# Optimization experiments

Measured on AMD Instinct MI355X. Metric: run time of the kernel, lower is better.

## Reference

```python
import jax, jax.numpy as jnp
import numpy as np
import math

B, N, D, H = 8, 1024, 512, 8
DH = D // H  # 64
FF = 4 * D   # 2048
SQRT_2_OVER_PI = math.sqrt(2.0 / math.pi)
LN_EPS = 1e-12


def gelu_new(x):
    # tanh-approx GELU as in DenseGatedGeluDense.gelu_new
    return 0.5 * x * (1.0 + jnp.tanh(SQRT_2_OVER_PI * (x + 0.044715 * x ** 3)))


def layer_norm(x, scale, bias):
    m = jnp.mean(x, axis=-1, keepdims=True)
    v = jnp.mean((x - m) ** 2, axis=-1, keepdims=True)
    return (x - m) * jax.lax.rsqrt(v + LN_EPS) * scale + bias


def setup_inputs() -> dict:
    key = jax.random.key(0)
    ks = jax.random.split(key, 12)
    w = lambda k, shape: (jax.random.normal(k, shape, jnp.float32) * 0.02)
    return {
        "X": jax.random.normal(ks[0], (B, N, D), jnp.float32),
        "train_ind": jax.random.randint(ks[1], (B, N), 0, 2).astype(jnp.int32),
        "batch_ind": jax.random.randint(ks[2], (B, N), 0, 2).astype(jnp.int32),
        "Wq": w(ks[3], (D, D)), "bq": jnp.zeros((D,), jnp.float32),
        "Wk": w(ks[4], (D, D)), "bk": jnp.zeros((D,), jnp.float32),
        "Wv": w(ks[5], (D, D)), "bv": jnp.zeros((D,), jnp.float32),
        "Wmix": w(ks[6], (D, D)), "bmix": jnp.zeros((D,), jnp.float32),
        "ln0_s": jnp.ones((D,), jnp.float32), "ln0_b": jnp.zeros((D,), jnp.float32),
        "ln1_s": jnp.ones((D,), jnp.float32), "ln1_b": jnp.zeros((D,), jnp.float32),
        "wi0": w(ks[7], (D, FF)),
        "wi1": w(ks[8], (D, FF)),
        "wo": w(ks[9], (FF, D)),
    }


def reference(X, train_ind, batch_ind, Wq, bq, Wk, bk, Wv, bv, Wmix, bmix,
              ln0_s, ln0_b, ln1_s, ln1_b, wi0, wi1, wo):
    # --- MAB with self-attention (SAB: Y = X), pre-LayerNorm variant ---
    Xn = layer_norm(X, ln0_s, ln0_b)          # ln0 applied to query side only
    Q = Xn @ Wq + bq                           # (B, N, D)
    X_res = Q                                  # fc_res is None -> residual = Q
    K = X @ Wk + bk                            # K/V computed from raw Y (=X)
    V = X @ Wv + bv

    Qh = Q.reshape(B, N, H, DH)
    Kh = K.reshape(B, N, H, DH)
    Vh = V.reshape(B, N, H, DH)

    # scores scaled by sqrt(dim_KV) per att_score_norm == 'softmax'
    scores = jnp.einsum("bqhd,bkhd->bhqk", Qh, Kh) / math.sqrt(D)  # (B,H,N,N)

    # get_attention_mask: key j attendable iff j in train or batch set, or j == i
    allowed_key = (train_ind + batch_ind) != 0                     # (B, N)
    allow = allowed_key[:, None, :] | jnp.eye(N, dtype=bool)[None] # (B, N, N)
    scores = jnp.where(allow[:, None, :, :], scores, -jnp.inf)

    A = jax.nn.softmax(scores, axis=-1)
    O = jnp.einsum("bhqk,bkhd->bqhd", A, Vh).reshape(B, N, D)

    Hc = O @ Wmix + bmix                       # fc_mix_heads
    Hc = X_res + Hc                            # residual (pre-LN branch)

    # GEGLU rFF block (DenseGatedGeluDense), pre-LN
    x1 = layer_norm(Hc, ln1_s, ln1_b)
    ff = (gelu_new(x1 @ wi0) * (x1 @ wi1)) @ wo
    return Hc + ff
```

## Files before the change

### kernel.cpp

```cpp
#include <hip/hip_runtime.h>
#include <hip/hip_bf16.h>
#include <math.h>

#define DEV __device__ __forceinline__

using bf16x8 = __attribute__((ext_vector_type(8))) short;
using f32x4  = __attribute__((ext_vector_type(4))) float;

static constexpr int Bb = 8, Nn = 1024, Dd = 512, Hh = 8, DHd = 64, FFd = 2048;
static constexpr int Mrows = Bb * Nn;

DEV short f2bf(float f) {
  union { float f; unsigned u; } v; v.f = f;
  unsigned r = v.u + 0x7fffu + ((v.u >> 16) & 1u);
  return (short)(r >> 16);
}
DEV float bf2f(short s) {
  union { unsigned u; float f; } v; v.u = ((unsigned)(unsigned short)s) << 16;
  return v.f;
}

DEV f32x4 mfma16(bf16x8 a, bf16x8 b, f32x4 c) {
  return __builtin_amdgcn_mfma_f32_16x16x32_bf16(a, b, c, 0, 0, 0);
}

DEV size_t swz(int r, int k, int ld) {
  return (size_t)(r >> 6) * 64 * ld + (size_t)(k >> 3) * 512
       + (size_t)((r & 63) * 8 + (k & 7));
}

DEV void gload16(const void* g, void* l) {
  __builtin_amdgcn_global_load_lds(
      (const __attribute__((address_space(1))) void*)g,
      (__attribute__((address_space(3))) void*)l, 16, 0, 0);
}

DEV float gelu_fast(float g) {
  float u2 = 1.5957691216057308f * (g + 0.044715f * g * g * g);
  return g / (1.0f + __expf(-u2));
}

DEV void xcd_tile(int gx, int gy, int& trow, int& tcol) {
  int wg = blockIdx.y * gx + blockIdx.x;
  int xcd = wg & 7, idx = wg >> 3;
  int XC = (gx >= 16) ? 2 : 1, XR = 8 / XC;
  int lcx = gx / XC, lcy = gy / XR;
  trow = (xcd / XC) * lcy + idx / lcx;
  tcol = (xcd % XC) * lcx + idx % lcx;
}

struct TJob { const float* src; short* dst; };
struct TJobs { TJob j[4]; };
__global__ __launch_bounds__(256)
void k_transpose_bf16(TJobs jobs, int K, int N) {
  const float* W = jobs.j[blockIdx.z].src;
  short* WT = jobs.j[blockIdx.z].dst;
  __shared__ float tile[32][33];
  int nb = blockIdx.x * 32, kb = blockIdx.y * 32;
  int tx = threadIdx.x & 31, ty = threadIdx.x >> 5;
  #pragma unroll
  for (int i = ty; i < 32; i += 8)
    tile[i][tx] = W[(size_t)(kb + i) * N + nb + tx];
  __syncthreads();
  #pragma unroll
  for (int i = ty; i < 32; i += 8)
    WT[swz(nb + i, kb + tx, K)] = f2bf(tile[tx][i]);
}

__global__ __launch_bounds__(256)
void k_mask(const int* __restrict__ train, const int* __restrict__ batch,
            char* __restrict__ allowC) {
  int i = blockIdx.x * 256 + threadIdx.x;
  allowC[i] = ((train[i] | batch[i]) != 0) ? 1 : 0;
}

template<bool WRITE_RAW>
__global__ __launch_bounds__(256)
void k_layernorm(const float* __restrict__ X, const float* __restrict__ sc,
                 const float* __restrict__ bi, short* __restrict__ out,
                 short* __restrict__ raw) {
  int w = threadIdx.x >> 6, lane = threadIdx.x & 63;
  int row = blockIdx.x * 4 + w;
  const float* x = X + (size_t)row * Dd + lane * 8;
  f32x4 a = *(const f32x4*)x;
  f32x4 b = *(const f32x4*)(x + 4);
  float p = a[0] + a[1] + a[2] + a[3] + b[0] + b[1] + b[2] + b[3];
  #pragma unroll
  for (int off = 1; off < 64; off <<= 1) p += __shfl_xor(p, off);
  float mean = p * (1.0f / Dd);
  float d[8];
  #pragma unroll
  for (int j = 0; j < 4; j++) { d[j] = a[j] - mean; d[4 + j] = b[j] - mean; }
  float q = 0.0f;
  #pragma unroll
  for (int j = 0; j < 8; j++) q += d[j] * d[j];
  #pragma unroll
  for (int off = 1; off < 64; off <<= 1) q += __shfl_xor(q, off);
  float rs = rsqrtf(q * (1.0f / Dd) + 1e-12f);
  int c0 = lane * 8;
  f32x4 s0 = *(const f32x4*)(sc + c0), s1 = *(const f32x4*)(sc + c0 + 4);
  f32x4 b0 = *(const f32x4*)(bi + c0), b1 = *(const f32x4*)(bi + c0 + 4);
  bf16x8 o;
  #pragma unroll
  for (int j = 0; j < 4; j++) {
    o[j]     = f2bf(d[j] * rs * s0[j] + b0[j]);
    o[4 + j] = f2bf(d[4 + j] * rs * s1[j] + b1[j]);
  }
  *(bf16x8*)(out + swz(row, c0, Dd)) = o;
  if (WRITE_RAW) {
    bf16x8 rv;
    #pragma unroll
    for (int j = 0; j < 4; j++) { rv[j] = f2bf(a[j]); rv[4 + j] = f2bf(b[j]); }
    *(bf16x8*)(raw + swz(row, c0, Dd)) = rv;
  }
}

template<int BN, int BK, int BIASM, int RESM, bool WF, bool WB, int EPI>
__global__ __launch_bounds__(256, 4)
void k_gemm128(const short* __restrict__ A, const short* __restrict__ BT,
               const float* __restrict__ bias, const float* __restrict__ resF,
               const short* __restrict__ resB, const short* __restrict__ gpre,
               float* __restrict__ outF, short* __restrict__ outB,
               int M, int N, int K) {
  constexpr int FN = BN / 32;
  __shared__ short lA[2][128 * BK];
  __shared__ short lB[2][BN * BK];
  int tid = threadIdx.x, w = tid >> 6, lane = tid & 63;
  int lr = lane & 15, lg = lane >> 4;
  int wr = w >> 1, wc = w & 1;
  int trow, tcol;
  xcd_tile(gridDim.x, gridDim.y, trow, tcol);
  int row0 = trow * 128, col0 = tcol * BN;
  f32x4 acc[4][FN] = {};

  auto stage = [&](int buf, int k0) {
    #pragma unroll
    for (int i = 0; i < BK / 16; i++) {
      int c = i * 4 + w;
      gload16(A + swz(row0 + (c & 1) * 64 + lane, k0 + (c >> 1) * 8, K),
              &lA[buf][c * 512]);
    }
    #pragma unroll
    for (int i = 0; i < (BN * BK) / 2048; i++) {
      int c = i * 4 + w;
      if (BN == 128)
        gload16(BT + swz(col0 + (c & 1) * 64 + lane, k0 + (c >> 1) * 8, K),
                &lB[buf][c * 512]);
      else
        gload16(BT + swz(col0 + lane, k0 + c * 8, K), &lB[buf][c * 512]);
    }
  };

  stage(0, 0);
  __syncthreads();
  int nt = K / BK, buf = 0;
  for (int t = 0; t < nt; t++) {
    if (t + 1 < nt) stage(buf ^ 1, (t + 1) * BK);
    #pragma unroll
    for (int kk = 0; kk < BK / 32; kk++) {
      bf16x8 af[4];
      #pragma unroll
      for (int m = 0; m < 4; m++)
        af[m] = *(const bf16x8*)&lA[buf][(kk * 4 + lg) * 1024 + (wr * 64 + m * 16 + lr) * 8];
      #pragma unroll
      for (int n = 0; n < FN; n++) {
        bf16x8 bfr = *(const bf16x8*)&lB[buf][(kk * 4 + lg) * (BN * 8)
                                              + (wc * (BN / 2) + n * 16 + lr) * 8];
        #pragma unroll
        for (int m = 0; m < 4; m++)
          acc[m][n] = mfma16(af[m], bfr, acc[m][n]);
      }
    }
    __syncthreads();
    buf ^= 1;
  }

  #pragma unroll
  for (int n = 0; n < FN; n++) {
    int col = col0 + wc * (BN / 2) + n * 16 + lr;
    float bv = (BIASM == 1) ? bias[col] : 0.0f;
    #pragma unroll
    for (int m = 0; m < 4; m++) {
      #pragma unroll
      for (int r = 0; r < 4; r++) {
        int rowg = row0 + wr * 64 + m * 16 + lg * 4 + r;
        float vv = acc[m][n][r] + bv;
        if (BIASM == 2) vv += bias[rowg];
        if (RESM == 1) vv += resF[(size_t)rowg * N + col];
        if (RESM == 2) vv += bf2f(resB[swz(rowg, col, N)]);
        if (EPI == 1) vv = gelu_fast(vv);
        if (EPI == 2) vv *= bf2f(gpre[swz(rowg, col, N)]);
        if (WF) outF[(size_t)rowg * N + col] = vv;
        if (WB) outB[swz(rowg, col, N)] = f2bf(vv);
      }
    }
  }
}

__global__ __launch_bounds__(256, 2)
void k_attention(const short* __restrict__ Qbf, const short* __restrict__ Kbf,
                 const short* __restrict__ VT, const char* __restrict__ allowC,
                 short* __restrict__ Obf) {
  __shared__ __align__(16) short Plds[4][32][72];
  __shared__ float maskF[Nn];
  int bid = blockIdx.x;
  int h = bid & 7, b = (bid >> 3) & 7, qt = bid >> 6;
  int tid = threadIdx.x, w = tid >> 6, lane = tid & 63, lr = lane & 15, lg = lane >> 4;
  int q0 = qt * 128 + w * 32;

  {
    const char* ac = allowC + b * Nn;
    #pragma unroll
    for (int j = 0; j < 4; j++) {
      int i = tid * 4 + j;
      maskF[i] = ac[i] ? 0.0f : -1e30f;
    }
  }
  __syncthreads();

  bf16x8 aq[2][2];
  #pragma unroll
  for (int qi = 0; qi < 2; qi++) {
    #pragma unroll
    for (int j = 0; j < 2; j++)
      aq[qi][j] = *(const bf16x8*)(Qbf + swz(b * Nn + q0 + qi * 16 + lr,
                                             h * 64 + j * 32 + lg * 8, Dd));
  }
  f32x4 acco[2][4] = {};
  float m_run[2][4], l_run[2][4];
  #pragma unroll
  for (int qi = 0; qi < 2; qi++)
  #pragma unroll
  for (int r = 0; r < 4; r++) { m_run[qi][r] = 0.0f; l_run[qi][r] = 0.0f; }
  const float scale = 0.044194173824159216f;

  auto loadK = [&](bf16x8 (&kf)[4][2], int kb) {
    #pragma unroll
    for (int sub = 0; sub < 4; sub++)
    #pragma unroll
    for (int j = 0; j < 2; j++)
      kf[sub][j] = *(const bf16x8*)(Kbf + swz(b * Nn + kb + sub * 16 + lr,
                                              h * 64 + j * 32 + lg * 8, Dd));
  };

  auto process = [&](bf16x8 (&kf)[4][2], int kb, bf16x8 (&kfn)[4][2], int kbn) {
    loadK(kfn, kbn);
    bf16x8 vb[2][4];
    #pragma unroll
    for (int ks = 0; ks < 2; ks++)
    #pragma unroll
    for (int t = 0; t < 4; t++)
      vb[ks][t] = *(const bf16x8*)(VT + swz(h * 64 + t * 16 + lr,
                                            b * Nn + kb + ks * 32 + lg * 8, Mrows));
    f32x4 accs[2][4] = {};
    #pragma unroll
    for (int sub = 0; sub < 4; sub++) {
      #pragma unroll
      for (int qi = 0; qi < 2; qi++) {
        accs[qi][sub] = mfma16(aq[qi][0], kf[sub][0], accs[qi][sub]);
        accs[qi][sub] = mfma16(aq[qi][1], kf[sub][1], accs[qi][sub]);
      }
    }
    float mk[4];
    #pragma unroll
    for (int sub = 0; sub < 4; sub++) mk[sub] = maskF[kb + sub * 16 + lr];
    float sv[2][4][4];
    #pragma unroll
    for (int qi = 0; qi < 2; qi++)
    #pragma unroll
    for (int sub = 0; sub < 4; sub++)
    #pragma unroll
    for (int r = 0; r < 4; r++)
      sv[qi][sub][r] = accs[qi][sub][r] * scale + mk[sub];
    if (kb == (q0 & ~63)) {
      #pragma unroll
      for (int qi = 0; qi < 2; qi++)
      #pragma unroll
      for (int sub = 0; sub < 4; sub++) {
        int key = kb + sub * 16 + lr;
        #pragma unroll
        for (int r = 0; r < 4; r++) {
          int qrow = q0 + qi * 16 + lg * 4 + r;
          if (key == qrow) sv[qi][sub][r] = accs[qi][sub][r] * scale;
        }
      }
    }
    bool allok = true;
    float pmax[2][4];
    #pragma unroll
    for (int qi = 0; qi < 2; qi++)
    #pragma unroll
    for (int r = 0; r < 4; r++) {
      pmax[qi][r] = fmaxf(fmaxf(sv[qi][0][r], sv[qi][1][r]),
                          fmaxf(sv[qi][2][r], sv[qi][3][r]));
      allok = allok && (pmax[qi][r] <= m_run[qi][r] + 8.0f);
    }
    if (!__all(allok)) {
      #pragma unroll
      for (int qi = 0; qi < 2; qi++)
      #pragma unroll
      for (int r = 0; r < 4; r++) {
        float m = pmax[qi][r];
        #pragma unroll
        for (int off = 1; off < 16; off <<= 1) m = fmaxf(m, __shfl_xor(m, off));
        float mtot = fmaxf(m_run[qi][r], m);
        float alpha = __expf(m_run[qi][r] - mtot);
        l_run[qi][r] *= alpha;
        m_run[qi][r] = mtot;
        #pragma unroll
        for (int t = 0; t < 4; t++) acco[qi][t][r] *= alpha;
      }
    }
    #pragma unroll
    for (int qi = 0; qi < 2; qi++) {
      #pragma unroll
      for (int sub = 0; sub < 4; sub++)
      #pragma unroll
      for (int r = 0; r < 4; r++) {
        float e = __expf(sv[qi][sub][r] - m_run[qi][r]);
        l_run[qi][r] += e;
        Plds[w][qi * 16 + lg * 4 + r][sub * 16 + lr] = f2bf(e);
      }
    }
    #pragma unroll
    for (int ks = 0; ks < 2; ks++) {
      bf16x8 pa0 = *(const bf16x8*)(&Plds[w][lr][ks * 32 + lg * 8]);
      bf16x8 pa1 = *(const bf16x8*)(&Plds[w][16 + lr][ks * 32 + lg * 8]);
      #pragma unroll
      for (int t = 0; t < 4; t++) {
        acco[0][t] = mfma16(pa0, vb[ks][t], acco[0][t]);
        acco[1][t] = mfma16(pa1, vb[ks][t], acco[1][t]);
      }
    }
  };

  bf16x8 kfA[4][2], kfB[4][2];
  loadK(kfA, 0);
  for (int kb = 0; kb < Nn; kb += 128) {
    int n1 = kb + 64;
    int n2 = (kb + 128 < Nn) ? (kb + 128) : 0;
    process(kfA, kb, kfB, n1);
    process(kfB, n1, kfA, n2);
  }

  #pragma unroll
  for (int qi = 0; qi < 2; qi++)
  #pragma unroll
  for (int r = 0; r < 4; r++) {
    float lsum = l_run[qi][r];
    #pragma unroll
    for (int off = 1; off < 16; off <<= 1) lsum += __shfl_xor(lsum, off);
    l_run[qi][r] = lsum;
  }
  #pragma unroll
  for (int qi = 0; qi < 2; qi++)
  #pragma unroll
  for (int t = 0; t < 4; t++)
  #pragma unroll
  for (int r = 0; r < 4; r++) {
    int q = b * Nn + q0 + qi * 16 + lg * 4 + r;
    Obf[swz(q, h * 64 + t * 16 + lr, Dd)] = f2bf(acco[qi][t][r] / l_run[qi][r]);
  }
}

extern "C" void kernel_launch(void* const* d_in, const int* in_sizes, int n_in,
                              void* d_out, int out_size, void* d_ws, size_t ws_size,
                              hipStream_t stream) {
  const float* X    = (const float*)d_in[0];
  const int*   train= (const int*)d_in[1];
  const int*   batch= (const int*)d_in[2];
  const float* Wq   = (const float*)d_in[3];
  const float* bq   = (const float*)d_in[4];
  const float* Wk   = (const float*)d_in[5];
  const float* bk   = (const float*)d_in[6];
  const float* Wv   = (const float*)d_in[7];
  const float* bv   = (const float*)d_in[8];
  const float* Wmix = (const float*)d_in[9];
  const float* bmix = (const float*)d_in[10];
  const float* ln0s = (const float*)d_in[11];
  const float* ln0b = (const float*)d_in[12];
  const float* ln1s = (const float*)d_in[13];
  const float* ln1b = (const float*)d_in[14];
  const float* wi0  = (const float*)d_in[15];
  const float* wi1  = (const float*)d_in[16];
  const float* wo   = (const float*)d_in[17];
  float* out = (float*)d_out;

  char* ws = (char*)d_ws;
  size_t off = 0;
  auto alloc = [&](size_t bytes) {
    off = (off + 255) & ~(size_t)255;
    void* p = ws + off; off += bytes; return p;
  };
  short* Xbf   = (short*)alloc((size_t)Mrows * Dd * 2);
  short* Xnbf  = (short*)alloc((size_t)Mrows * Dd * 2);
  short* Qbf   = (short*)alloc((size_t)Mrows * Dd * 2);
  short* Kbf   = (short*)alloc((size_t)Mrows * Dd * 2);
  short* VTg   = (short*)alloc((size_t)Dd * Mrows * 2);
  short* Obf   = (short*)alloc((size_t)Mrows * Dd * 2);
  short* x1bf  = (short*)alloc((size_t)Mrows * Dd * 2);
  short* Gbf   = (short*)alloc((size_t)Mrows * FFd * 2);
  short* FFbf  = (short*)alloc((size_t)Mrows * FFd * 2);
  short* WqT   = (short*)alloc((size_t)Dd * Dd * 2);
  short* WkT   = (short*)alloc((size_t)Dd * Dd * 2);
  short* WvT   = (short*)alloc((size_t)Dd * Dd * 2);
  short* WmixT = (short*)alloc((size_t)Dd * Dd * 2);
  short* wi0T  = (short*)alloc((size_t)FFd * Dd * 2);
  short* wi1T  = (short*)alloc((size_t)FFd * Dd * 2);
  short* woT   = (short*)alloc((size_t)Dd * FFd * 2);
  float* Hcf   = (float*)alloc((size_t)Mrows * Dd * 4);
  char*  allowC= (char*)alloc((size_t)Mrows);

  dim3 blk(256);
  TJobs tj4; tj4.j[0] = {Wq, WqT}; tj4.j[1] = {Wk, WkT};
  tj4.j[2] = {Wv, WvT}; tj4.j[3] = {Wmix, WmixT};
  k_transpose_bf16<<<dim3(Dd / 32, Dd / 32, 4), blk, 0, stream>>>(tj4, Dd, Dd);
  TJobs tj2; tj2.j[0] = {wi0, wi0T}; tj2.j[1] = {wi1, wi1T};
  tj2.j[2] = {wi0, wi0T}; tj2.j[3] = {wi1, wi1T};
  k_transpose_bf16<<<dim3(FFd / 32, Dd / 32, 2), blk, 0, stream>>>(tj2, Dd, FFd);
  TJobs tj1; tj1.j[0] = {wo, woT}; tj1.j[1] = {wo, woT};
  tj1.j[2] = {wo, woT}; tj1.j[3] = {wo, woT};
  k_transpose_bf16<<<dim3(Dd / 32, FFd / 32, 1), blk, 0, stream>>>(tj1, FFd, Dd);

  k_mask<<<Mrows / 256, blk, 0, stream>>>(train, batch, allowC);

  k_layernorm<true><<<Mrows / 4, blk, 0, stream>>>(X, ln0s, ln0b, Xnbf, Xbf);

  k_gemm128<64, 64, 1, 0, false, true, 0><<<dim3(Dd / 64, Mrows / 128), blk, 0, stream>>>(
      Xnbf, WqT, bq, nullptr, nullptr, nullptr, nullptr, Qbf, Mrows, Dd, Dd);
  k_gemm128<64, 64, 1, 0, false, true, 0><<<dim3(Dd / 64, Mrows / 128), blk, 0, stream>>>(
      Xbf, WkT, bk, nullptr, nullptr, nullptr, nullptr, Kbf, Mrows, Dd, Dd);
  k_gemm128<64, 64, 2, 0, false, true, 0><<<dim3(Mrows / 64, Dd / 128), blk, 0, stream>>>(
      WvT, Xbf, bv, nullptr, nullptr, nullptr, nullptr, VTg, Dd, Mrows, Dd);

  k_attention<<<Bb * Hh * (Nn / 128), blk, 0, stream>>>(Qbf, Kbf, VTg, allowC, Obf);

  k_gemm128<64, 64, 1, 2, true, false, 0><<<dim3(Dd / 64, Mrows / 128), blk, 0, stream>>>(
      Obf, WmixT, bmix, nullptr, Qbf, nullptr, Hcf, nullptr, Mrows, Dd, Dd);

  k_layernorm<false><<<Mrows / 4, blk, 0, stream>>>(Hcf, ln1s, ln1b, x1bf, nullptr);

  k_gemm128<128, 32, 0, 0, false, true, 1><<<dim3(FFd / 128, Mrows / 128), blk, 0, stream>>>(
      x1bf, wi0T, nullptr, nullptr, nullptr, nullptr, nullptr, Gbf, Mrows, FFd, Dd);
  k_gemm128<128, 32, 0, 0, false, true, 2><<<dim3(FFd / 128, Mrows / 128), blk, 0, stream>>>(
      x1bf, wi1T, nullptr, nullptr, nullptr, Gbf, nullptr, FFbf, Mrows, FFd, Dd);

  k_gemm128<64, 64, 0, 1, true, false, 0><<<dim3(Dd / 64, Mrows / 128), blk, 0, stream>>>(
      FFbf, woT, nullptr, Hcf, nullptr, nullptr, out, nullptr, Mrows, Dd, FFd);
}
```

Before: 207.5 us.

## Halve attention query tile per wave, double grid, use exp2 in softmax and GELU

Each attention wave now handles 16 query rows instead of 32, so the block covers 64 queries, the grid doubles and launch bounds request 4 blocks per CU for higher occupancy. The softmax scale is folded into a log2e-scaled constant so the exponentials use the native exp2 instruction, with the rescale threshold adjusted to match. GELU also switches to exp2 with a pre-multiplied constant. The cost is that each K/V fragment loaded from global memory is reused by half as many query rows, roughly doubling K/V load traffic in attention.

```diff
diff --git a/kernel.cpp b/kernel.cpp
--- a/kernel.cpp
+++ b/kernel.cpp
@@ -19,6 +19,7 @@
   union { unsigned u; float f; } v; v.u = ((unsigned)(unsigned short)s) << 16;
   return v.f;
 }
+DEV float fexp2(float x) { return __builtin_amdgcn_exp2f(x); }
 
 DEV f32x4 mfma16(bf16x8 a, bf16x8 b, f32x4 c) {
   return __builtin_amdgcn_mfma_f32_16x16x32_bf16(a, b, c, 0, 0, 0);
@@ -36,8 +37,8 @@
 }
 
 DEV float gelu_fast(float g) {
-  float u2 = 1.5957691216057308f * (g + 0.044715f * g * g * g);
-  return g / (1.0f + __expf(-u2));
+  float u2l = 2.30220822f * (g + 0.044715f * g * g * g);
+  return g / (1.0f + fexp2(-u2l));
 }
 
 DEV void xcd_tile(int gx, int gy, int& trow, int& tcol) {
@@ -197,16 +198,16 @@
   }
 }
 
-__global__ __launch_bounds__(256, 2)
+__global__ __launch_bounds__(256, 4)
 void k_attention(const short* __restrict__ Qbf, const short* __restrict__ Kbf,
                  const short* __restrict__ VT, const char* __restrict__ allowC,
                  short* __restrict__ Obf) {
-  __shared__ __align__(16) short Plds[4][32][72];
+  __shared__ __align__(16) short Plds[4][16][72];
   __shared__ float maskF[Nn];
   int bid = blockIdx.x;
   int h = bid & 7, b = (bid >> 3) & 7, qt = bid >> 6;
   int tid = threadIdx.x, w = tid >> 6, lane = tid & 63, lr = lane & 15, lg = lane >> 4;
-  int q0 = qt * 128 + w * 32;
+  int q0 = qt * 64 + w * 16;
 
   {
     const char* ac = allowC + b * Nn;
@@ -218,21 +219,16 @@
   }
   __syncthreads();
 
-  bf16x8 aq[2][2];
-  #pragma unroll
-  for (int qi = 0; qi < 2; qi++) {
-    #pragma unroll
-    for (int j = 0; j < 2; j++)
-      aq[qi][j] = *(const bf16x8*)(Qbf + swz(b * Nn + q0 + qi * 16 + lr,
-                                             h * 64 + j * 32 + lg * 8, Dd));
-  }
-  f32x4 acco[2][4] = {};
-  float m_run[2][4], l_run[2][4];
-  #pragma unroll
-  for (int qi = 0; qi < 2; qi++)
-  #pragma unroll
-  for (int r = 0; r < 4; r++) { m_run[qi][r] = 0.0f; l_run[qi][r] = 0.0f; }
-  const float scale = 0.044194173824159216f;
+  bf16x8 aq[2];
+  #pragma unroll
+  for (int j = 0; j < 2; j++)
+    aq[j] = *(const bf16x8*)(Qbf + swz(b * Nn + q0 + lr,
+                                       h * 64 + j * 32 + lg * 8, Dd));
+  f32x4 acco[4] = {};
+  float m_run[4], l_run[4];
+  #pragma unroll
+  for (int r = 0; r < 4; r++) { m_run[r] = 0.0f; l_run[r] = 0.0f; }
+  const float scale2 = 0.06375871573f;
 
   auto loadK = [&](bf16x8 (&kf)[4][2], int kb) {
     #pragma unroll
@@ -252,85 +248,67 @@
     for (int t = 0; t < 4; t++)
       vb[ks][t] = *(const bf16x8*)(VT + swz(h * 64 + t * 16 + lr,
                                             b * Nn + kb + ks * 32 + lg * 8, Mrows));
-    f32x4 accs[2][4] = {};
+    f32x4 accs[4] = {};
     #pragma unroll
     for (int sub = 0; sub < 4; sub++) {
-      #pragma unroll
-      for (int qi = 0; qi < 2; qi++) {
-        accs[qi][sub] = mfma16(aq[qi][0], kf[sub][0], accs[qi][sub]);
-        accs[qi][sub] = mfma16(aq[qi][1], kf[sub][1], accs[qi][sub]);
-      }
+      accs[sub] = mfma16(aq[0], kf[sub][0], accs[sub]);
+      accs[sub] = mfma16(aq[1], kf[sub][1], accs[sub]);
     }
     float mk[4];
     #pragma unroll
     for (int sub = 0; sub < 4; sub++) mk[sub] = maskF[kb + sub * 16 + lr];
-    float sv[2][4][4];
-    #pragma unroll
-    for (int qi = 0; qi < 2; qi++)
+    float sv[4][4];
     #pragma unroll
     for (int sub = 0; sub < 4; sub++)
     #pragma unroll
     for (int r = 0; r < 4; r++)
-      sv[qi][sub][r] = accs[qi][sub][r] * scale + mk[sub];
+      sv[sub][r] = accs[sub][r] * scale2 + mk[sub];
     if (kb == (q0 & ~63)) {
-      #pragma unroll
-      for (int qi = 0; qi < 2; qi++)
       #pragma unroll
       for (int sub = 0; sub < 4; sub++) {
         int key = kb + sub * 16 + lr;
         #pragma unroll
         for (int r = 0; r < 4; r++) {
-          int qrow = q0 + qi * 16 + lg * 4 + r;
-          if (key == qrow) sv[qi][sub][r] = accs[qi][sub][r] * scale;
+          int qrow = q0 + lg * 4 + r;
+          if (key == qrow) sv[sub][r] = accs[sub][r] * scale2;
         }
       }
     }
     bool allok = true;
-    float pmax[2][4];
-    #pragma unroll
-    for (int qi = 0; qi < 2; qi++)
+    float pmax[4];
     #pragma unroll
     for (int r = 0; r < 4; r++) {
-      pmax[qi][r] = fmaxf(fmaxf(sv[qi][0][r], sv[qi][1][r]),
-                          fmaxf(sv[qi][2][r], sv[qi][3][r]));
-      allok = allok && (pmax[qi][r] <= m_run[qi][r] + 8.0f);
+      pmax[r] = fmaxf(fmaxf(sv[0][r], sv[1][r]), fmaxf(sv[2][r], sv[3][r]));
+      allok = allok && (pmax[r] <= m_run[r] + 11.5416f);
     }
     if (!__all(allok)) {
       #pragma unroll
-      for (int qi = 0; qi < 2; qi++)
-      #pragma unroll
       for (int r = 0; r < 4; r++) {
-        float m = pmax[qi][r];
+        float m = pmax[r];
         #pragma unroll
         for (int off = 1; off < 16; off <<= 1) m = fmaxf(m, __shfl_xor(m, off));
-        float mtot = fmaxf(m_run[qi][r], m);
-        float alpha = __expf(m_run[qi][r] - mtot);
-        l_run[qi][r] *= alpha;
-        m_run[qi][r] = mtot;
+        float mtot = fmaxf(m_run[r], m);
+        float alpha = fexp2(m_run[r] - mtot);
+        l_run[r] *= alpha;
+        m_run[r] = mtot;
         #pragma unroll
-        for (int t = 0; t < 4; t++) acco[qi][t][r] *= alpha;
+        for (int t = 0; t < 4; t++) acco[t][r] *= alpha;
       }
     }
     #pragma unroll
-    for (int qi = 0; qi < 2; qi++) {
-      #pragma unroll
-      for (int sub = 0; sub < 4; sub++)
-      #pragma unroll
-      for (int r = 0; r < 4; r++) {
-        float e = __expf(sv[qi][sub][r] - m_run[qi][r]);
-        l_run[qi][r] += e;
-        Plds[w][qi * 16 + lg * 4 + r][sub * 16 + lr] = f2bf(e);
-      }
+    for (int sub = 0; sub < 4; sub++)
+    #pragma unroll
+    for (int r = 0; r < 4; r++) {
+      float e = fexp2(sv[sub][r] - m_run[r]);
+      l_run[r] += e;
+      Plds[w][lg * 4 + r][sub * 16 + lr] = f2bf(e);
     }
     #pragma unroll
     for (int ks = 0; ks < 2; ks++) {
-      bf16x8 pa0 = *(const bf16x8*)(&Plds[w][lr][ks * 32 + lg * 8]);
-      bf16x8 pa1 = *(const bf16x8*)(&Plds[w][16 + lr][ks * 32 + lg * 8]);
-      #pragma unroll
-      for (int t = 0; t < 4; t++) {
-        acco[0][t] = mfma16(pa0, vb[ks][t], acco[0][t]);
-        acco[1][t] = mfma16(pa1, vb[ks][t], acco[1][t]);
-      }
+      bf16x8 pa = *(const bf16x8*)(&Plds[w][lr][ks * 32 + lg * 8]);
+      #pragma unroll
+      for (int t = 0; t < 4; t++)
+        acco[t] = mfma16(pa, vb[ks][t], acco[t]);
     }
   };
 
@@ -344,22 +322,18 @@
   }
 
   #pragma unroll
-  for (int qi = 0; qi < 2; qi++)
-  #pragma unroll
   for (int r = 0; r < 4; r++) {
-    float lsum = l_run[qi][r];
+    float lsum = l_run[r];
     #pragma unroll
     for (int off = 1; off < 16; off <<= 1) lsum += __shfl_xor(lsum, off);
-    l_run[qi][r] = lsum;
-  }
-  #pragma unroll
-  for (int qi = 0; qi < 2; qi++)
+    l_run[r] = lsum;
+  }
   #pragma unroll
   for (int t = 0; t < 4; t++)
   #pragma unroll
   for (int r = 0; r < 4; r++) {
-    int q = b * Nn + q0 + qi * 16 + lg * 4 + r;
-    Obf[swz(q, h * 64 + t * 16 + lr, Dd)] = f2bf(acco[qi][t][r] / l_run[qi][r]);
+    int q = b * Nn + q0 + lg * 4 + r;
+    Obf[swz(q, h * 64 + t * 16 + lr, Dd)] = f2bf(acco[t][r] / l_run[r]);
   }
 }
 
@@ -433,7 +407,7 @@
   k_gemm128<64, 64, 2, 0, false, true, 0><<<dim3(Mrows / 64, Dd / 128), blk, 0, stream>>>(
       WvT, Xbf, bv, nullptr, nullptr, nullptr, nullptr, VTg, Dd, Mrows, Dd);
 
-  k_attention<<<Bb * Hh * (Nn / 128), blk, 0, stream>>>(Qbf, Kbf, VTg, allowC, Obf);
+  k_attention<<<Bb * Hh * (Nn / 64), blk, 0, stream>>>(Qbf, Kbf, VTg, allowC, Obf);
 
   k_gemm128<64, 64, 1, 2, true, false, 0><<<dim3(Dd / 64, Mrows / 128), blk, 0, stream>>>(
       Obf, WmixT, bmix, nullptr, Qbf, nullptr, Hcf, nullptr, Mrows, Dd, Dd);
```

Result: slower. 356.9 us (+72.0%).
